# Kernel optimization log

Measured on AMD Instinct MI355X. Metric: run time of the kernel, lower is better.

The kernel has to match this reference:

```python
import jax, jax.numpy as jnp
import numpy as np

N, V, H, K = 65536, 200, 128, 32

def _corr_cols(a, B):
    # Pearson correlation between vector a [M] and each column of B [M, V]
    ac = a - a.mean()
    Bc = B - B.mean(axis=0)
    num = (ac[:, None] * Bc).sum(axis=0)
    den = jnp.sqrt((ac ** 2).sum() * (Bc ** 2).sum(axis=0))
    return jnp.nan_to_num(num / den, nan=0.0)

def _pairwise_features(tv, ti, cv, ci):
    # tv, ti: [N]; cv, ci: [N, V] -> features [V, 11]
    tvc = tv[:, None]
    both = (1.0 - ti)[:, None] * (1.0 - ci)
    n = both.sum(0) + 1e-8
    tmean = (tvc * both).sum(0) / n
    cmean = (cv * both).sum(0) / n
    tcent = (tvc - tmean) * both
    ccent = (cv - cmean) * both
    cov = (tcent * ccent).sum(0) / n
    tstd = jnp.sqrt((tcent ** 2).sum(0) / n + 1e-8)
    cstd = jnp.sqrt((ccent ** 2).sum(0) / n + 1e-8)
    corr = cov / (tstd * cstd + 1e-8)
    mi = -0.5 * jnp.log(1.0 - jnp.minimum(corr ** 2, 0.99) + 1e-8)
    tmin, tmax = tv.min(), tv.max()
    cmin, cmax = cv.min(0), cv.max(0)
    overlap = jnp.maximum(0.0, (jnp.minimum(tmax, cmax) - jnp.maximum(tmin, cmin)) / (jnp.maximum(tmax - tmin, cmax - cmin) + 1e-8))
    lag = _corr_cols(tv[1:], cv[:-1])       # corrcoef(candidate[:-1], target[1:])
    rev = _corr_cols(tv[:-1], cv[1:])       # corrcoef(target[:-1], candidate[1:])
    var_t = jnp.var(tv)
    coef = corr * jnp.std(tv) / (cv.std(0) + 1e-8)
    residual = tvc - coef * (cv - cv.mean(0))
    var_ratio = residual.var(0) / (var_t + 1e-8)
    intv = (ci > 0.5).astype(tv.dtype)
    t_int = (tvc * intv).sum(0) / (intv.sum(0) + 1e-8)
    t_no = (tvc * (1.0 - intv)).sum(0) / ((1.0 - intv).sum(0) + 1e-8)
    effect = jnp.abs(t_int - t_no)
    tr = jnp.argsort(jnp.argsort(tv)).astype(tv.dtype)
    cr = jnp.argsort(jnp.argsort(cv, axis=0), axis=0).astype(tv.dtype)
    rank_corr = _corr_cols(tr, cr)
    feats = jnp.stack([corr, jnp.abs(corr), corr ** 2, mi, overlap, effect,
                       rank_corr, jnp.sign(corr), lag, rev, var_ratio], axis=-1)
    return jnp.nan_to_num(feats, nan=0.0)

def _forward(target_embedding, node_embeddings, data, W_pair, b_pair, Wq, bq, Wk, bk,
             W1, b1, ln_scale, ln_offset, W2, b2, W3, b3, Wd, target_idx):
    n_vars = node_embeddings.shape[0]
    tv, ti = data[:, target_idx, 0], data[:, target_idx, 1]
    cv, ci = data[:, :, 0], data[:, :, 1]
    pf = _pairwise_features(tv, ti, cv, ci)                       # [V, 11]
    pf = jnp.where((jnp.arange(n_vars) == target_idx)[:, None], 0.0, pf)
    q = target_embedding @ Wq + bq                                # [K]
    k = node_embeddings @ Wk + bk + (pf @ W_pair + b_pair)        # [V, K]
    scores = (k @ q) / jnp.sqrt(jnp.asarray(float(K), dtype=q.dtype))
    te = jnp.broadcast_to(target_embedding, (n_vars, target_embedding.shape[0]))
    combined = jnp.concatenate([te, node_embeddings, pf * 10.0], axis=-1)  # [V, 2H+11]
    h = jax.nn.gelu(combined @ W1 + b1)
    mu = h.mean(-1, keepdims=True)
    var = ((h - mu) ** 2).mean(-1, keepdims=True)
    h = (h - mu) / jnp.sqrt(var + 1e-5) * ln_scale + ln_offset    # LayerNorm (haiku eps=1e-5)
    h = jax.nn.gelu(h @ W2 + b2)
    net = (h @ W3 + b3)[:, 0]
    direct = (pf[:, jnp.array([0, 8, 10])] @ Wd)[:, 0]
    return scores + net + 0.5 * direct

def setup_inputs():
    key = jax.random.key(0)
    ks = jax.random.split(key, 16)
    def vs_uniform(k, fan_in, shape):
        # hk.initializers.VarianceScaling(2.0, 'fan_in', 'uniform')
        lim = np.sqrt(6.0 / fan_in)
        return jax.random.uniform(k, shape, minval=-lim, maxval=lim, dtype=jnp.float32)
    vals = jax.random.normal(ks[0], (N, V), dtype=jnp.float32)
    intv = (jax.random.uniform(ks[1], (N, V)) < 0.1).astype(jnp.float32)
    data = jnp.stack([vals, intv, jnp.ones((N, V), jnp.float32)], axis=-1)  # [N, V, 3]
    return {
        'target_embedding': jax.random.normal(ks[2], (H,), dtype=jnp.float32),
        'node_embeddings': jax.random.normal(ks[3], (V, H), dtype=jnp.float32),
        'data': data,
        'W_pair': vs_uniform(ks[4], 11, (11, K)), 'b_pair': jnp.zeros((K,), jnp.float32),
        'Wq': vs_uniform(ks[5], H, (H, K)), 'bq': jnp.zeros((K,), jnp.float32),
        'Wk': vs_uniform(ks[6], H, (H, K)), 'bk': jnp.zeros((K,), jnp.float32),
        'W1': vs_uniform(ks[7], 2 * H + 11, (2 * H + 11, H)), 'b1': jnp.zeros((H,), jnp.float32),
        'ln_scale': jnp.ones((H,), jnp.float32), 'ln_offset': jnp.zeros((H,), jnp.float32),
        'W2': vs_uniform(ks[8], H, (H, H // 2)), 'b2': jnp.zeros((H // 2,), jnp.float32),
        'W3': vs_uniform(ks[9], H // 2, (H // 2, 1)), 'b3': jnp.zeros((1,), jnp.float32),
        'Wd': vs_uniform(ks[10], 3, (3, 1)),
        'target_idx': 0,
    }

def reference(target_embedding, node_embeddings, data, W_pair, b_pair, Wq, bq, Wk, bk,
              W1, b1, ln_scale, ln_offset, W2, b2, W3, b3, Wd, target_idx):
    return _forward(target_embedding, node_embeddings, data, W_pair, b_pair, Wq, bq, Wk, bk,
                    W1, b1, ln_scale, ln_offset, W2, b2, W3, b3, Wd, target_idx)
```

## Files before the change

kernel.cpp:

```cpp
#include <hip/hip_runtime.h>
#include <stdint.h>

#define N_ROWS 65536
#define NV 200
#define NH 128
#define NKD 32
#define NBKT 32768
#define ROWS_B 32
#define NB2A (N_ROWS/ROWS_B)

__device__ __forceinline__ uint32_t fkey(float x){
  uint32_t u = __float_as_uint(x);
  return (u & 0x80000000u) ? ~u : (u | 0x80000000u);
}

__global__ __launch_bounds__(256) void k_extract(
    const float* __restrict__ data, const int* __restrict__ tgt,
    float* __restrict__ tvArr, float* __restrict__ tiArr,
    unsigned int* __restrict__ histT, double* __restrict__ tvP){
  int i = blockIdx.x*256 + threadIdx.x;
  int tg = *tgt;
  float v  = data[(size_t)i*600 + tg*3 + 0];
  float ti = data[(size_t)i*600 + tg*3 + 1];
  tvArr[i] = v; tiArr[i] = ti;
  atomicAdd(&histT[fkey(v)>>17], 1u);
  double s = (double)v, ss = (double)v*(double)v;
  float mn = v, mx = v;
  for (int off=32; off; off>>=1){
    s  += __shfl_down(s,  off);
    ss += __shfl_down(ss, off);
    mn = fminf(mn, __shfl_down(mn, off));
    mx = fmaxf(mx, __shfl_down(mx, off));
  }
  __shared__ double sd[4][4];
  int w = threadIdx.x >> 6;
  if ((threadIdx.x & 63) == 0){ sd[w][0]=s; sd[w][1]=ss; sd[w][2]=mn; sd[w][3]=mx; }
  __syncthreads();
  if (threadIdx.x == 0){
    double S=0, SS=0, MN=sd[0][2], MX=sd[0][3];
    for (int q=0;q<4;q++){ S+=sd[q][0]; SS+=sd[q][1]; MN=fmin(MN,sd[q][2]); MX=fmax(MX,sd[q][3]); }
    double* p = tvP + (size_t)blockIdx.x*4;
    p[0]=S; p[1]=SS; p[2]=MN; p[3]=MX;
  }
}

__global__ __launch_bounds__(256) void k_comb_tv(const double* __restrict__ tvP,
                                                 double* __restrict__ tvStats){
  int t = threadIdx.x;
  double s = tvP[t*4+0], ss = tvP[t*4+1], mn = tvP[t*4+2], mx = tvP[t*4+3];
  for (int off=32; off; off>>=1){
    s  += __shfl_down(s,  off);
    ss += __shfl_down(ss, off);
    mn = fmin(mn, __shfl_down(mn, off));
    mx = fmax(mx, __shfl_down(mx, off));
  }
  __shared__ double sd[4][4];
  int w = t >> 6;
  if ((t & 63) == 0){ sd[w][0]=s; sd[w][1]=ss; sd[w][2]=mn; sd[w][3]=mx; }
  __syncthreads();
  if (t == 0){
    double S=0, SS=0, MN=sd[0][2], MX=sd[0][3];
    for (int q=0;q<4;q++){ S+=sd[q][0]; SS+=sd[q][1]; MN=fmin(MN,sd[q][2]); MX=fmax(MX,sd[q][3]); }
    tvStats[0]=S; tvStats[1]=SS; tvStats[2]=MN; tvStats[3]=MX;
  }
}

__global__ __launch_bounds__(256) void k_scan(unsigned int* __restrict__ histT){
  __shared__ unsigned int h[256*129];
  __shared__ unsigned int aux[256];
  int t = threadIdx.x;
  for (int idx=t; idx<NBKT; idx+=256) h[(idx>>7)*129 + (idx&127)] = histT[idx];
  __syncthreads();
  unsigned int s = 0;
  #pragma unroll 8
  for (int k=0;k<128;k++) s += h[t*129+k];
  aux[t] = s; __syncthreads();
  for (int off=1; off<256; off<<=1){
    unsigned int v = (t>=off) ? aux[t-off] : 0u;
    __syncthreads();
    aux[t] += v;
    __syncthreads();
  }
  unsigned int run = aux[t] - s;
  #pragma unroll 8
  for (int k=0;k<128;k++){
    unsigned int c = h[t*129+k];
    h[t*129+k] = __float_as_uint((float)run + 0.5f*((float)c - 1.f));
    run += c;
  }
  __syncthreads();
  for (int idx=t; idx<NBKT; idx+=256) histT[idx] = h[(idx>>7)*129 + (idx&127)];
}

__global__ __launch_bounds__(256) void k_trank(const float* __restrict__ tvArr,
                                               const unsigned int* __restrict__ histT,
                                               float* __restrict__ trArr){
  int i = blockIdx.x*256 + threadIdx.x;
  trArr[i] = __uint_as_float(histT[fkey(tvArr[i])>>17]);
}

__global__ __launch_bounds__(256, 4) void k_main(
    const float* __restrict__ data, const float* __restrict__ tvArr,
    const float* __restrict__ tiArr, uint16_t* __restrict__ bktT,
    float* __restrict__ colP){
  __shared__ float   cvS[ROWS_B][201];
  __shared__ uint8_t ciS[ROWS_B][204];
  __shared__ float   tvS[ROWS_B+2];
  __shared__ float   tiS[ROWS_B];
  int t = threadIdx.x, blk = blockIdx.x;
  int i0 = blk*ROWS_B;

  const float4* rb = (const float4*)(data + (size_t)i0*600);
  float4 vals[19];
  #pragma unroll
  for (int k=0;k<18;k++) vals[k] = rb[t + k*256];
  if (t < 192) vals[18] = rb[t + 18*256];
  if (t < ROWS_B+2){ int i = i0 - 1 + t; tvS[t] = (i>=0 && i<N_ROWS) ? tvArr[i] : 0.f; }
  else if (t >= 64 && t < 64+ROWS_B){ tiS[t-64] = tiArr[i0 + (t-64)]; }

  #pragma unroll
  for (int k=0;k<19;k++){
    int f = t + k*256;
    if (k < 18 || t < 192){
      float4 v = vals[k];
      int r  = f/150;
      int e4 = f - r*150;
      int m  = e4 % 3;
      int c0 = (4*e4)/3;
      if (m==0){ cvS[r][c0]=v.x; ciS[r][c0]=(uint8_t)(v.y>0.5f); cvS[r][c0+1]=v.w; }
      else if (m==1){ ciS[r][c0]=(uint8_t)(v.x>0.5f); cvS[r][c0+1]=v.z; ciS[r][c0+1]=(uint8_t)(v.w>0.5f); }
      else { cvS[r][c0+1]=v.y; ciS[r][c0+1]=(uint8_t)(v.z>0.5f); }
    }
  }
  __syncthreads();

  if (t < NV){
    float facc[13];
    #pragma unroll
    for (int s=0;s<13;s++) facc[s]=0.f;
    float cmin = 3.4e38f, cmax = -3.4e38f;
    for (int r=0;r<ROWS_B;r++){
      float cv = cvS[r][t];
      float ci = (float)ciS[r][t];
      float tv = tvS[r+1], tvm = tvS[r], tvp = tvS[r+2];
      float ti = tiS[r];
      float b  = (1.f-ti)*(1.f-ci);
      facc[0]+=cv;        facc[1]+=cv*cv;     facc[2]+=tv*cv;
      facc[3]+=ci;        facc[4]+=tv*ci;
      facc[5]+=b;         facc[6]+=tv*b;      facc[7]+=cv*b;
      facc[8]+=tv*cv*b;   facc[9]+=tv*tv*b;   facc[10]+=cv*cv*b;
      facc[11]+=tvp*cv;   facc[12]+=tvm*cv;
      cmin = fminf(cmin, cv); cmax = fmaxf(cmax, cv);
    }
    float* dst = colP + ((size_t)t*NB2A + blk)*16;
    #pragma unroll
    for (int s=0;s<13;s++) dst[s] = facc[s];
    dst[13]=cmin; dst[14]=cmax;
  }

  {
    int r = t & 31, cb = t >> 5;
    for (int cc=cb; cc<NV; cc+=8){
      float cv = cvS[r][cc];
      bktT[(size_t)cc*N_ROWS + i0 + r] = (uint16_t)(fkey(cv)>>17);
    }
  }
}

__global__ __launch_bounds__(256) void k_comb_cols(const float* __restrict__ colP,
                                                   double* __restrict__ colStats){
  int j = blockIdx.x, t = threadIdx.x;
  double a[13];
  #pragma unroll
  for (int s=0;s<13;s++) a[s]=0.0;
  float mn = 3.4e38f, mx = -3.4e38f;
  for (int b=t; b<NB2A; b+=256){
    const float* p = colP + ((size_t)j*NB2A + b)*16;
    #pragma unroll
    for (int s=0;s<13;s++) a[s] += (double)p[s];
    mn = fminf(mn, p[13]); mx = fmaxf(mx, p[14]);
  }
  for (int off=32; off; off>>=1){
    #pragma unroll
    for (int s=0;s<13;s++) a[s] += __shfl_down(a[s], off);
    mn = fminf(mn, __shfl_down(mn, off));
    mx = fmaxf(mx, __shfl_down(mx, off));
  }
  __shared__ double sd[4][15];
  int w = t >> 6;
  if ((t & 63) == 0){
    #pragma unroll
    for (int s=0;s<13;s++) sd[w][s]=a[s];
    sd[w][13]=(double)mn; sd[w][14]=(double)mx;
  }
  __syncthreads();
  if (t == 0){
    double* d = colStats + (size_t)j*16;
    #pragma unroll
    for (int s=0;s<13;s++) d[s] = sd[0][s]+sd[1][s]+sd[2][s]+sd[3][s];
    double MN=sd[0][13], MX=sd[0][14];
    for (int q=1;q<4;q++){ MN=fmin(MN,sd[q][13]); MX=fmax(MX,sd[q][14]); }
    d[13]=MN; d[14]=MX;
  }
}

__global__ __launch_bounds__(512, 1) void k_rank(const uint16_t* __restrict__ bktT,
                                                 const float* __restrict__ trArr,
                                                 double* __restrict__ colStats){
  __shared__ unsigned int h[512*65];
  __shared__ unsigned int aux[512];
  __shared__ double daux[8];
  int t = threadIdx.x, j = blockIdx.x;
  const uint16_t* col = bktT + (size_t)j*N_ROWS;
  for (int idx=t; idx<512*65; idx+=512) h[idx]=0u;
  __syncthreads();
  for (int k=0;k<N_ROWS/512;k++){
    int b = (int)col[t + k*512];
    atomicAdd(&h[(b>>6)*65 + (b&63)], 1u);
  }
  __syncthreads();
  unsigned int s = 0;
  #pragma unroll 8
  for (int k=0;k<64;k++) s += h[t*65+k];
  aux[t]=s; __syncthreads();
  for (int off=1; off<512; off<<=1){
    unsigned int v = (t>=off) ? aux[t-off] : 0u;
    __syncthreads();
    aux[t] += v;
    __syncthreads();
  }
  unsigned int run = aux[t] - s;
  #pragma unroll 8
  for (int k=0;k<64;k++){
    unsigned int c = h[t*65+k];
    h[t*65+k] = __float_as_uint((float)run + 0.5f*((float)c - 1.f));
    run += c;
  }
  __syncthreads();
  double srr = 0.0;
  for (int k=0;k<N_ROWS/512;k++){
    int i = t + k*512;
    int b = (int)col[i];
    srr += (double)trArr[i] * (double)__uint_as_float(h[(b>>6)*65 + (b&63)]);
  }
  for (int off=32; off; off>>=1) srr += __shfl_down(srr, off);
  if ((t&63)==0) daux[t>>6] = srr;
  __syncthreads();
  if (t==0){
    double s8=0;
    for (int q=0;q<8;q++) s8 += daux[q];
    colStats[(size_t)j*16 + 15] = s8;
  }
}

__device__ __forceinline__ float gelu_t(float x){
  float x3 = x*x*x;
  return 0.5f*x*(1.f + tanhf(0.7978845608f*(x + 0.044715f*x3)));
}

__global__ __launch_bounds__(128) void k_head(
    const float* __restrict__ te, const float* __restrict__ ne, const float* __restrict__ data,
    const float* __restrict__ Wpair, const float* __restrict__ bpair,
    const float* __restrict__ Wq, const float* __restrict__ bq,
    const float* __restrict__ Wk, const float* __restrict__ bk,
    const float* __restrict__ W1, const float* __restrict__ b1,
    const float* __restrict__ lns, const float* __restrict__ lno,
    const float* __restrict__ W2, const float* __restrict__ b2,
    const float* __restrict__ W3, const float* __restrict__ b3,
    const float* __restrict__ Wd, const int* __restrict__ tgt,
    const double* __restrict__ colStats, const double* __restrict__ tvStats,
    const float* __restrict__ tvArr, float* __restrict__ out){
  int j = blockIdx.x, t = threadIdx.x;
  int tg = *tgt;
  const double* cs = colStats + (size_t)j*16;
  double S_c=cs[0], S_cc=cs[1], S_tc=cs[2], S_ci=cs[3], S_ti=cs[4], S_b=cs[5],
         S_tb=cs[6], S_cb=cs[7], S_tcb=cs[8], S_ttb=cs[9], S_ccb=cs[10], L=cs[11], R=cs[12];
  float cmin=(float)cs[13], cmax=(float)cs[14];
  double S_rr=cs[15];
  double S_t=tvStats[0], S_tt=tvStats[1];
  float tmin=(float)tvStats[2], tmax=(float)tvStats[3];
  float tv0=tvArr[0], tvN=tvArr[N_ROWS-1];
  float cv0=data[j*3], cvN=data[(size_t)(N_ROWS-1)*600 + j*3];
  const double Nd = (double)N_ROWS;
  double n = S_b + 1e-8;
  double tmean=S_tb/n, cmean=S_cb/n;
  double cov=(S_tcb - tmean*S_cb - cmean*S_tb + tmean*cmean*S_b)/n;
  double t2=S_ttb - 2.0*tmean*S_tb + tmean*tmean*S_b;
  double c2=S_ccb - 2.0*cmean*S_cb + cmean*cmean*S_b;
  double tstd=sqrt(t2/n + 1e-8), cstd=sqrt(c2/n + 1e-8);
  double corr = cov/(tstd*cstd + 1e-8);
  double mi = -0.5*log(1.0 - fmin(corr*corr, 0.99) + 1e-8);
  float ovn = fminf(tmax,cmax) - fmaxf(tmin,cmin);
  float ovd = fmaxf(tmax-tmin, cmax-cmin) + 1e-8f;
  float overlap = fmaxf(0.f, ovn/ovd);
  double M = Nd - 1.0;
  double Sa=S_t-(double)tv0, Saa=S_tt-(double)tv0*(double)tv0;
  double Sb2=S_c-(double)cvN, Sbb=S_cc-(double)cvN*(double)cvN;
  double lnum = L - Sa*Sb2/M;
  double lden2 = (Saa - Sa*Sa/M)*(Sbb - Sb2*Sb2/M);
  double lag = (lden2 > 0.0) ? lnum/sqrt(lden2) : 0.0;
  double Sa2=S_t-(double)tvN, Saa2=S_tt-(double)tvN*(double)tvN;
  double Sc2=S_c-(double)cv0, Scc2=S_cc-(double)cv0*(double)cv0;
  double rnum = R - Sa2*Sc2/M;
  double rden2 = (Saa2 - Sa2*Sa2/M)*(Scc2 - Sc2*Sc2/M);
  double rev = (rden2 > 0.0) ? rnum/sqrt(rden2) : 0.0;
  double var_t = S_tt/Nd - (S_t/Nd)*(S_t/Nd);
  double var_c = S_cc/Nd - (S_c/Nd)*(S_c/Nd);
  double coef = corr*sqrt(var_t)/(sqrt(var_c) + 1e-8);
  double covf = S_tc/Nd - (S_t/Nd)*(S_c/Nd);
  double var_res = var_t + coef*coef*var_c - 2.0*coef*covf;
  double var_ratio = var_res/(var_t + 1e-8);
  double t_int = S_ti/(S_ci + 1e-8);
  double t_no  = (S_t - S_ti)/((Nd - S_ci) + 1e-8);
  double effect = fabs(t_int - t_no);
  const double m_ = (Nd-1.0)*0.5;
  double rank_corr = (S_rr - Nd*m_*m_) / (Nd*(Nd*Nd-1.0)/12.0);
  float pf[11];
  pf[0]=(float)corr; pf[1]=(float)fabs(corr); pf[2]=(float)(corr*corr); pf[3]=(float)mi;
  pf[4]=overlap; pf[5]=(float)effect; pf[6]=(float)rank_corr;
  pf[7]=(float)((corr>0.0)-(corr<0.0)); pf[8]=(float)lag; pf[9]=(float)rev; pf[10]=(float)var_ratio;
  if (j == tg){
    #pragma unroll
    for (int q=0;q<11;q++) pf[q]=0.f;
  }
  const float* nej = ne + (size_t)j*NH;
  float h = b1[t];
  for (int e=0;e<NH;e++) h += te[e]*W1[e*NH + t];
  for (int e=0;e<NH;e++) h += nej[e]*W1[(NH+e)*NH + t];
  #pragma unroll
  for (int f=0;f<11;f++) h += 10.f*pf[f]*W1[(2*NH+f)*NH + t];
  h = gelu_t(h);
  __shared__ float redW[2];
  __shared__ float hnS[NH];
  __shared__ float h2S[64];
  float v = h;
  for (int off=32; off; off>>=1) v += __shfl_down(v, off);
  if ((t&63)==0) redW[t>>6]=v;
  __syncthreads();
  float mu = (redW[0]+redW[1])*(1.f/128.f);
  __syncthreads();
  float d = h - mu;
  v = d*d;
  for (int off=32; off; off>>=1) v += __shfl_down(v, off);
  if ((t&63)==0) redW[t>>6]=v;
  __syncthreads();
  float var = (redW[0]+redW[1])*(1.f/128.f);
  float hn = d/sqrtf(var + 1e-5f)*lns[t] + lno[t];
  hnS[t] = hn;
  __syncthreads();
  if (t < 64){
    float h2 = b2[t];
    for (int o=0;o<NH;o++) h2 += hnS[o]*W2[o*64 + t];
    h2S[t] = gelu_t(h2);
  }
  __syncthreads();
  float netv = 0.f, scv = 0.f;
  if (t < 64){
    float v2 = h2S[t]*W3[t];
    for (int off=32; off; off>>=1) v2 += __shfl_down(v2, off);
    if (t==0) netv = v2 + b3[0];
  }
  if (t < 32){
    float q = bq[t], k = bk[t] + bpair[t];
    for (int e=0;e<NH;e++){ q += te[e]*Wq[e*NKD + t]; k += nej[e]*Wk[e*NKD + t]; }
    #pragma unroll
    for (int f=0;f<11;f++) k += pf[f]*Wpair[f*NKD + t];
    float sc = k*q;
    for (int off=16; off; off>>=1) sc += __shfl_down(sc, off, 32);
    if (t==0) scv = sc/sqrtf(32.f);
  }
  if (t == 0){
    float direct = pf[0]*Wd[0] + pf[8]*Wd[1] + pf[10]*Wd[2];
    out[j] = scv + netv + 0.5f*direct;
  }
}

extern "C" void kernel_launch(void* const* d_in, const int* in_sizes, int n_in,
                              void* d_out, int out_size, void* d_ws, size_t ws_size,
                              hipStream_t stream) {
  const float* te    = (const float*)d_in[0];
  const float* ne    = (const float*)d_in[1];
  const float* data  = (const float*)d_in[2];
  const float* Wpair = (const float*)d_in[3];
  const float* bpair = (const float*)d_in[4];
  const float* Wq    = (const float*)d_in[5];
  const float* bq    = (const float*)d_in[6];
  const float* Wk    = (const float*)d_in[7];
  const float* bk    = (const float*)d_in[8];
  const float* W1    = (const float*)d_in[9];
  const float* b1    = (const float*)d_in[10];
  const float* lns   = (const float*)d_in[11];
  const float* lno   = (const float*)d_in[12];
  const float* W2    = (const float*)d_in[13];
  const float* b2    = (const float*)d_in[14];
  const float* W3    = (const float*)d_in[15];
  const float* b3    = (const float*)d_in[16];
  const float* Wd    = (const float*)d_in[17];
  const int*   tgt   = (const int*)d_in[18];
  float* out = (float*)d_out;

  char* ws = (char*)d_ws;
  size_t off = 0;
  auto alloc = [&](size_t bytes)->char*{
    char* p = ws + off;
    off = (off + bytes + 255) & ~(size_t)255;
    return p;
  };
  uint16_t*     bktT     = (uint16_t*)    alloc((size_t)NV*N_ROWS*2);
  float*        tvArr    = (float*)       alloc(N_ROWS*4);
  float*        tiArr    = (float*)       alloc(N_ROWS*4);
  float*        trArr    = (float*)       alloc(N_ROWS*4);
  unsigned int* histT    = (unsigned int*)alloc(NBKT*4);
  double*       tvP      = (double*)      alloc(256*4*8);
  double*       tvStats  = (double*)      alloc(4*8);
  float*        colP     = (float*)       alloc((size_t)NV*NB2A*16*4);
  double*       colStats = (double*)      alloc((size_t)NV*16*8);
  if (off > ws_size) return;

  hipMemsetAsync(histT, 0, NBKT*4, stream);
  k_extract<<<dim3(N_ROWS/256), dim3(256), 0, stream>>>(data, tgt, tvArr, tiArr, histT, tvP);
  k_comb_tv<<<dim3(1), dim3(256), 0, stream>>>(tvP, tvStats);
  k_scan<<<dim3(1), dim3(256), 0, stream>>>(histT);
  k_trank<<<dim3(N_ROWS/256), dim3(256), 0, stream>>>(tvArr, histT, trArr);
  k_main<<<dim3(NB2A), dim3(256), 0, stream>>>(data, tvArr, tiArr, bktT, colP);
  k_comb_cols<<<dim3(NV), dim3(256), 0, stream>>>(colP, colStats);
  k_rank<<<dim3(NV), dim3(512), 0, stream>>>(bktT, trArr, colStats);
  k_head<<<dim3(NV), dim3(128), 0, stream>>>(te, ne, data, Wpair, bpair, Wq, bq, Wk, bk,
                                             W1, b1, lns, lno, W2, b2, W3, b3, Wd, tgt,
                                             colStats, tvStats, tvArr, out);
}
```

Before: 410.6 us.

## Fuse small kernels, restructure k_main to per-thread column loads, widen k_rank

Drops k_comb_tv and k_trank. The target-stats reduction moves into k_head, and the target rank lookup moves into k_rank. k_main is rewritten so each thread reads its own column directly with float2 loads, over 64 rows per block in 16-row chunks, instead of staging through shared memory. It writes the bucket keys as 16-byte vector stores. k_rank now uses 1024 threads with a smaller per-thread histogram. The goal is fewer launches and better write coalescing, at the cost of strided uncoalesced global reads in k_main and redundant tvP reduction work in every k_head block.

```diff
diff --git a/kernel.cpp b/kernel.cpp
--- a/kernel.cpp
+++ b/kernel.cpp
@@ -6,8 +6,8 @@
 #define NH 128
 #define NKD 32
 #define NBKT 32768
-#define ROWS_B 32
-#define NB2A (N_ROWS/ROWS_B)
+#define ROWS_B 64
+#define NBLK (N_ROWS/ROWS_B)
 
 __device__ __forceinline__ uint32_t fkey(float x){
   uint32_t u = __float_as_uint(x);
@@ -44,27 +44,6 @@
   }
 }
 
-__global__ __launch_bounds__(256) void k_comb_tv(const double* __restrict__ tvP,
-                                                 double* __restrict__ tvStats){
-  int t = threadIdx.x;
-  double s = tvP[t*4+0], ss = tvP[t*4+1], mn = tvP[t*4+2], mx = tvP[t*4+3];
-  for (int off=32; off; off>>=1){
-    s  += __shfl_down(s,  off);
-    ss += __shfl_down(ss, off);
-    mn = fmin(mn, __shfl_down(mn, off));
-    mx = fmax(mx, __shfl_down(mx, off));
-  }
-  __shared__ double sd[4][4];
-  int w = t >> 6;
-  if ((t & 63) == 0){ sd[w][0]=s; sd[w][1]=ss; sd[w][2]=mn; sd[w][3]=mx; }
-  __syncthreads();
-  if (t == 0){
-    double S=0, SS=0, MN=sd[0][2], MX=sd[0][3];
-    for (int q=0;q<4;q++){ S+=sd[q][0]; SS+=sd[q][1]; MN=fmin(MN,sd[q][2]); MX=fmax(MX,sd[q][3]); }
-    tvStats[0]=S; tvStats[1]=SS; tvStats[2]=MN; tvStats[3]=MX;
-  }
-}
-
 __global__ __launch_bounds__(256) void k_scan(unsigned int* __restrict__ histT){
   __shared__ unsigned int h[256*129];
   __shared__ unsigned int aux[256];
@@ -92,78 +71,64 @@
   for (int idx=t; idx<NBKT; idx+=256) histT[idx] = h[(idx>>7)*129 + (idx&127)];
 }
 
-__global__ __launch_bounds__(256) void k_trank(const float* __restrict__ tvArr,
-                                               const unsigned int* __restrict__ histT,
-                                               float* __restrict__ trArr){
-  int i = blockIdx.x*256 + threadIdx.x;
-  trArr[i] = __uint_as_float(histT[fkey(tvArr[i])>>17]);
-}
-
 __global__ __launch_bounds__(256, 4) void k_main(
     const float* __restrict__ data, const float* __restrict__ tvArr,
     const float* __restrict__ tiArr, uint16_t* __restrict__ bktT,
     float* __restrict__ colP){
-  __shared__ float   cvS[ROWS_B][201];
-  __shared__ uint8_t ciS[ROWS_B][204];
-  __shared__ float   tvS[ROWS_B+2];
-  __shared__ float   tiS[ROWS_B];
   int t = threadIdx.x, blk = blockIdx.x;
   int i0 = blk*ROWS_B;
-
-  const float4* rb = (const float4*)(data + (size_t)i0*600);
-  float4 vals[19];
+  bool act = (t < NV);
+  const float* base = data + (size_t)i0*600 + t*3;
+  uint16_t* bout = bktT + (size_t)t*N_ROWS + i0;
+
+  float facc[13];
   #pragma unroll
-  for (int k=0;k<18;k++) vals[k] = rb[t + k*256];
-  if (t < 192) vals[18] = rb[t + 18*256];
-  if (t < ROWS_B+2){ int i = i0 - 1 + t; tvS[t] = (i>=0 && i<N_ROWS) ? tvArr[i] : 0.f; }
-  else if (t >= 64 && t < 64+ROWS_B){ tiS[t-64] = tiArr[i0 + (t-64)]; }
-
-  #pragma unroll
-  for (int k=0;k<19;k++){
-    int f = t + k*256;
-    if (k < 18 || t < 192){
-      float4 v = vals[k];
-      int r  = f/150;
-      int e4 = f - r*150;
-      int m  = e4 % 3;
-      int c0 = (4*e4)/3;
-      if (m==0){ cvS[r][c0]=v.x; ciS[r][c0]=(uint8_t)(v.y>0.5f); cvS[r][c0+1]=v.w; }
-      else if (m==1){ ciS[r][c0]=(uint8_t)(v.x>0.5f); cvS[r][c0+1]=v.z; ciS[r][c0+1]=(uint8_t)(v.w>0.5f); }
-      else { cvS[r][c0+1]=v.y; ciS[r][c0+1]=(uint8_t)(v.z>0.5f); }
+  for (int s=0;s<13;s++) facc[s]=0.f;
+  float cmin = 3.4e38f, cmax = -3.4e38f;
+
+  for (int c=0; c<4; ++c){
+    int r0 = i0 + c*16;
+    float2 v[16];
+    if (act){
+      #pragma unroll
+      for (int r=0;r<16;r++)
+        v[r] = *(const float2*)(base + (size_t)(c*16+r)*600);
     }
-  }
-  __syncthreads();
-
-  if (t < NV){
-    float facc[13];
-    #pragma unroll
-    for (int s=0;s<13;s++) facc[s]=0.f;
-    float cmin = 3.4e38f, cmax = -3.4e38f;
-    for (int r=0;r<ROWS_B;r++){
-      float cv = cvS[r][t];
-      float ci = (float)ciS[r][t];
-      float tv = tvS[r+1], tvm = tvS[r], tvp = tvS[r+2];
-      float ti = tiS[r];
-      float b  = (1.f-ti)*(1.f-ci);
-      facc[0]+=cv;        facc[1]+=cv*cv;     facc[2]+=tv*cv;
-      facc[3]+=ci;        facc[4]+=tv*ci;
-      facc[5]+=b;         facc[6]+=tv*b;      facc[7]+=cv*b;
-      facc[8]+=tv*cv*b;   facc[9]+=tv*tv*b;   facc[10]+=cv*cv*b;
-      facc[11]+=tvp*cv;   facc[12]+=tvm*cv;
-      cmin = fminf(cmin, cv); cmax = fmaxf(cmax, cv);
+    float tvv[18];
+    #pragma unroll
+    for (int k=0;k<18;k++){
+      int i = r0 + k - 1;
+      tvv[k] = (i>=0 && i<N_ROWS) ? tvArr[i] : 0.f;
     }
-    float* dst = colP + ((size_t)t*NB2A + blk)*16;
+    float tii[16];
+    #pragma unroll
+    for (int k=0;k<16;k++) tii[k] = tiArr[r0+k];
+
+    if (act){
+      uint16_t bb[16];
+      #pragma unroll
+      for (int r=0;r<16;r++){
+        float cv = v[r].x;
+        float ci = v[r].y;
+        float tv = tvv[r+1], tvm = tvv[r], tvp = tvv[r+2];
+        float b  = (1.f-tii[r])*(1.f-ci);
+        facc[0]+=cv;        facc[1]+=cv*cv;     facc[2]+=tv*cv;
+        facc[3]+=ci;        facc[4]+=tv*ci;
+        facc[5]+=b;         facc[6]+=tv*b;      facc[7]+=cv*b;
+        facc[8]+=tv*cv*b;   facc[9]+=tv*tv*b;   facc[10]+=cv*cv*b;
+        facc[11]+=tvp*cv;   facc[12]+=tvm*cv;
+        cmin = fminf(cmin, cv); cmax = fmaxf(cmax, cv);
+        bb[r] = (uint16_t)(fkey(cv)>>17);
+      }
+      *((uint4*)(bout + c*16))     = *((uint4*)(bb));
+      *((uint4*)(bout + c*16 + 8)) = *((uint4*)(bb + 8));
+    }
+  }
+  if (act){
+    float* dst = colP + ((size_t)t*NBLK + blk)*16;
     #pragma unroll
     for (int s=0;s<13;s++) dst[s] = facc[s];
     dst[13]=cmin; dst[14]=cmax;
-  }
-
-  {
-    int r = t & 31, cb = t >> 5;
-    for (int cc=cb; cc<NV; cc+=8){
-      float cv = cvS[r][cc];
-      bktT[(size_t)cc*N_ROWS + i0 + r] = (uint16_t)(fkey(cv)>>17);
-    }
   }
 }
 
@@ -174,8 +139,8 @@
   #pragma unroll
   for (int s=0;s<13;s++) a[s]=0.0;
   float mn = 3.4e38f, mx = -3.4e38f;
-  for (int b=t; b<NB2A; b+=256){
-    const float* p = colP + ((size_t)j*NB2A + b)*16;
+  for (int b=t; b<NBLK; b+=256){
+    const float* p = colP + ((size_t)j*NBLK + b)*16;
     #pragma unroll
     for (int s=0;s<13;s++) a[s] += (double)p[s];
     mn = fminf(mn, p[13]); mx = fmaxf(mx, p[14]);
@@ -204,26 +169,27 @@
   }
 }
 
-__global__ __launch_bounds__(512, 1) void k_rank(const uint16_t* __restrict__ bktT,
-                                                 const float* __restrict__ trArr,
-                                                 double* __restrict__ colStats){
-  __shared__ unsigned int h[512*65];
-  __shared__ unsigned int aux[512];
-  __shared__ double daux[8];
+__global__ __launch_bounds__(1024, 1) void k_rank(const uint16_t* __restrict__ bktT,
+                                                  const float* __restrict__ tvArr,
+                                                  const unsigned int* __restrict__ histT,
+                                                  double* __restrict__ colStats){
+  __shared__ unsigned int h[1024*33];
+  __shared__ unsigned int aux[1024];
+  __shared__ double daux[16];
   int t = threadIdx.x, j = blockIdx.x;
   const uint16_t* col = bktT + (size_t)j*N_ROWS;
-  for (int idx=t; idx<512*65; idx+=512) h[idx]=0u;
-  __syncthreads();
-  for (int k=0;k<N_ROWS/512;k++){
-    int b = (int)col[t + k*512];
-    atomicAdd(&h[(b>>6)*65 + (b&63)], 1u);
+  for (int idx=t; idx<1024*33; idx+=1024) h[idx]=0u;
+  __syncthreads();
+  for (int k=0;k<N_ROWS/1024;k++){
+    int b = (int)col[t + k*1024];
+    atomicAdd(&h[(b>>5)*33 + (b&31)], 1u);
   }
   __syncthreads();
   unsigned int s = 0;
   #pragma unroll 8
-  for (int k=0;k<64;k++) s += h[t*65+k];
+  for (int k=0;k<32;k++) s += h[t*33+k];
   aux[t]=s; __syncthreads();
-  for (int off=1; off<512; off<<=1){
+  for (int off=1; off<1024; off<<=1){
     unsigned int v = (t>=off) ? aux[t-off] : 0u;
     __syncthreads();
     aux[t] += v;
@@ -231,25 +197,26 @@
   }
   unsigned int run = aux[t] - s;
   #pragma unroll 8
-  for (int k=0;k<64;k++){
-    unsigned int c = h[t*65+k];
-    h[t*65+k] = __float_as_uint((float)run + 0.5f*((float)c - 1.f));
+  for (int k=0;k<32;k++){
+    unsigned int c = h[t*33+k];
+    h[t*33+k] = __float_as_uint((float)run + 0.5f*((float)c - 1.f));
     run += c;
   }
   __syncthreads();
   double srr = 0.0;
-  for (int k=0;k<N_ROWS/512;k++){
-    int i = t + k*512;
+  for (int k=0;k<N_ROWS/1024;k++){
+    int i = t + k*1024;
     int b = (int)col[i];
-    srr += (double)trArr[i] * (double)__uint_as_float(h[(b>>6)*65 + (b&63)]);
+    float tr = __uint_as_float(histT[fkey(tvArr[i])>>17]);
+    srr += (double)tr * (double)__uint_as_float(h[(b>>5)*33 + (b&31)]);
   }
   for (int off=32; off; off>>=1) srr += __shfl_down(srr, off);
   if ((t&63)==0) daux[t>>6] = srr;
   __syncthreads();
   if (t==0){
-    double s8=0;
-    for (int q=0;q<8;q++) s8 += daux[q];
-    colStats[(size_t)j*16 + 15] = s8;
+    double s16=0;
+    for (int q=0;q<16;q++) s16 += daux[q];
+    colStats[(size_t)j*16 + 15] = s16;
   }
 }
 
@@ -268,17 +235,37 @@
     const float* __restrict__ W2, const float* __restrict__ b2,
     const float* __restrict__ W3, const float* __restrict__ b3,
     const float* __restrict__ Wd, const int* __restrict__ tgt,
-    const double* __restrict__ colStats, const double* __restrict__ tvStats,
+    const double* __restrict__ colStats, const double* __restrict__ tvP,
     const float* __restrict__ tvArr, float* __restrict__ out){
   int j = blockIdx.x, t = threadIdx.x;
   int tg = *tgt;
+
+  __shared__ double tvsd[2][4];
+  {
+    double s  = tvP[t*4+0] + tvP[(t+128)*4+0];
+    double ss = tvP[t*4+1] + tvP[(t+128)*4+1];
+    double mn = fmin(tvP[t*4+2], tvP[(t+128)*4+2]);
+    double mx = fmax(tvP[t*4+3], tvP[(t+128)*4+3]);
+    for (int off=32; off; off>>=1){
+      s  += __shfl_down(s,  off);
+      ss += __shfl_down(ss, off);
+      mn = fmin(mn, __shfl_down(mn, off));
+      mx = fmax(mx, __shfl_down(mx, off));
+    }
+    int w = t>>6;
+    if ((t&63)==0){ tvsd[w][0]=s; tvsd[w][1]=ss; tvsd[w][2]=mn; tvsd[w][3]=mx; }
+    __syncthreads();
+  }
+  double S_t  = tvsd[0][0] + tvsd[1][0];
+  double S_tt = tvsd[0][1] + tvsd[1][1];
+  float tmin  = (float)fmin(tvsd[0][2], tvsd[1][2]);
+  float tmax  = (float)fmax(tvsd[0][3], tvsd[1][3]);
+
   const double* cs = colStats + (size_t)j*16;
   double S_c=cs[0], S_cc=cs[1], S_tc=cs[2], S_ci=cs[3], S_ti=cs[4], S_b=cs[5],
          S_tb=cs[6], S_cb=cs[7], S_tcb=cs[8], S_ttb=cs[9], S_ccb=cs[10], L=cs[11], R=cs[12];
   float cmin=(float)cs[13], cmax=(float)cs[14];
   double S_rr=cs[15];
-  double S_t=tvStats[0], S_tt=tvStats[1];
-  float tmin=(float)tvStats[2], tmax=(float)tvStats[3];
   float tv0=tvArr[0], tvN=tvArr[N_ROWS-1];
   float cv0=data[j*3], cvN=data[(size_t)(N_ROWS-1)*600 + j*3];
   const double Nd = (double)N_ROWS;
@@ -409,23 +396,19 @@
   uint16_t*     bktT     = (uint16_t*)    alloc((size_t)NV*N_ROWS*2);
   float*        tvArr    = (float*)       alloc(N_ROWS*4);
   float*        tiArr    = (float*)       alloc(N_ROWS*4);
-  float*        trArr    = (float*)       alloc(N_ROWS*4);
   unsigned int* histT    = (unsigned int*)alloc(NBKT*4);
   double*       tvP      = (double*)      alloc(256*4*8);
-  double*       tvStats  = (double*)      alloc(4*8);
-  float*        colP     = (float*)       alloc((size_t)NV*NB2A*16*4);
+  float*        colP     = (float*)       alloc((size_t)NV*NBLK*16*4);
   double*       colStats = (double*)      alloc((size_t)NV*16*8);
   if (off > ws_size) return;
 
   hipMemsetAsync(histT, 0, NBKT*4, stream);
   k_extract<<<dim3(N_ROWS/256), dim3(256), 0, stream>>>(data, tgt, tvArr, tiArr, histT, tvP);
-  k_comb_tv<<<dim3(1), dim3(256), 0, stream>>>(tvP, tvStats);
   k_scan<<<dim3(1), dim3(256), 0, stream>>>(histT);
-  k_trank<<<dim3(N_ROWS/256), dim3(256), 0, stream>>>(tvArr, histT, trArr);
-  k_main<<<dim3(NB2A), dim3(256), 0, stream>>>(data, tvArr, tiArr, bktT, colP);
+  k_main<<<dim3(NBLK), dim3(256), 0, stream>>>(data, tvArr, tiArr, bktT, colP);
   k_comb_cols<<<dim3(NV), dim3(256), 0, stream>>>(colP, colStats);
-  k_rank<<<dim3(NV), dim3(512), 0, stream>>>(bktT, trArr, colStats);
+  k_rank<<<dim3(NV), dim3(1024), 0, stream>>>(bktT, tvArr, histT, colStats);
   k_head<<<dim3(NV), dim3(128), 0, stream>>>(te, ne, data, Wpair, bpair, Wq, bq, Wk, bk,
                                              W1, b1, lns, lno, W2, b2, W3, b3, Wd, tgt,
-                                             colStats, tvStats, tvArr, out);
-}
+                                             colStats, tvP, tvArr, out);
+}
```

Result: slower. 434.2 us (+5.7%).
